# Performance work log

Hardware: AMD Instinct MI355X
Metric: run time of the kernel (lower is better)

The kernel has to match this reference:

```python
import jax, jax.numpy as jnp
import numpy as np


def setup_inputs() -> dict:
    key = jax.random.key(0)
    n_keypoints = 129          # n keypoints -> 128 segments
    spacing = 32               # uniform keypoint spacing -> m = 4096
    dim = 256
    batch = 32
    index = jnp.arange(n_keypoints, dtype=jnp.int64 if jax.config.jax_enable_x64 else jnp.int32) * spacing
    value = jax.random.normal(key, (batch, n_keypoints, dim), dtype=jnp.float32)
    return {"index": index, "value": value}


def reference(index, value):
    """Piecewise linear interpolation; vectorized over all segments/points.

    index: (n,) sorted keypoint positions (static values).
    value: (..., n, dim) keypoint values.
    returns: (..., m, dim) with m = index[-1] - index[0]; excludes the start point.
    """
    idx = index - index[0]                       # (n,) starts at 0
    m = int(np.asarray(idx)[-1])                 # static: index is a known tensor
    p = jnp.arange(1, m + 1)                     # output positions (m,)
    # segment k such that idx[k] < p <= idx[k+1]
    seg = jnp.searchsorted(idx, p, side="left") - 1   # (m,)
    x0 = idx[seg]                                # (m,)
    x1 = idx[seg + 1]                            # (m,)
    w = ((p - x0) / (x1 - x0)).astype(value.dtype)    # (m,) fractional position in segment
    y0 = value[..., seg, :]                      # (..., m, dim)
    y1 = value[..., seg + 1, :]                  # (..., m, dim)
    return y0 + (y1 - y0) * w[:, None]
```

## Files before the change

kernel.cpp:

```cpp
#include <hip/hip_runtime.h>
#include <hip/hip_bf16.h>


#define DIM 256
#define VEC_PER_ROW (DIM / 4)
#define MAX_N 256

__global__ __launch_bounds__(256) void lpi_kernel(
    const int* __restrict__ index,
    const float* __restrict__ value,
    float* __restrict__ out,
    int n, int m, int batch)
{
    __shared__ int s_idx[MAX_N];

    int base = index[0];
    for (int i = threadIdx.x; i < n; i += blockDim.x) {
        s_idx[i] = index[i] - base;
    }
    __syncthreads();

    int t = blockIdx.x * blockDim.x + threadIdx.x;
    int total = batch * m * VEC_PER_ROW;
    if (t >= total) return;

    int dv  = t & (VEC_PER_ROW - 1);
    int row = t >> 6;
    int r   = row % m;
    int b   = row / m;
    int p   = r + 1;

    int lo = 0, hi = n - 1;
    while (lo < hi) {
        int mid = (lo + hi + 1) >> 1;
        if (s_idx[mid] < p) lo = mid; else hi = mid - 1;
    }
    int seg = lo;

    int x0 = s_idx[seg];
    int x1 = s_idx[seg + 1];
    float w = (float)(p - x0) / (float)(x1 - x0);

    const float4* y0 = (const float4*)(value + (size_t)(b * n + seg) * DIM);
    const float4* y1 = y0 + VEC_PER_ROW;

    float4 a = y0[dv];
    float4 c = y1[dv];

    float4 o;
    o.x = a.x + (c.x - a.x) * w;
    o.y = a.y + (c.y - a.y) * w;
    o.z = a.z + (c.z - a.z) * w;
    o.w = a.w + (c.w - a.w) * w;

    float4* op = (float4*)(out + (size_t)(b * m + r) * DIM);
    op[dv] = o;
}

extern "C" void kernel_launch(void* const* d_in, const int* in_sizes, int n_in,
                              void* d_out, int out_size, void* d_ws, size_t ws_size,
                              hipStream_t stream) {
    const int*   index = (const int*)d_in[0];
    const float* value = (const float*)d_in[1];
    float*       out   = (float*)d_out;

    int n  = in_sizes[0];
    int bd = in_sizes[1] / n;
    const int dim = DIM;
    int batch = bd / dim;
    int m = out_size / bd;

    int total = batch * m * VEC_PER_ROW;
    int block = 256;
    int grid  = (total + block - 1) / block;

    lpi_kernel<<<grid, block, 0, stream>>>(index, value, out, n, m, batch);
}
```

Measured before the change: 162.5 us.

## Map blocks to segments, drop binary search, reuse keypoint rows with nontemporal stores

Each block now owns one (batch, segment) pair and loops over all output rows in that segment. It loads the two keypoint rows once per block and skips the per-thread binary search and the shared-memory index staging. Output is written with nontemporal stores to avoid polluting the cache. Parallelism per block now depends on segment length, so very uneven keypoint spacing could cause load imbalance.

```diff
diff --git a/kernel.cpp b/kernel.cpp
--- a/kernel.cpp
+++ b/kernel.cpp
@@ -4,57 +4,42 @@
 
 #define DIM 256
 #define VEC_PER_ROW (DIM / 4)
-#define MAX_N 256
+
+typedef float vfloat4 __attribute__((ext_vector_type(4)));
 
 __global__ __launch_bounds__(256) void lpi_kernel(
     const int* __restrict__ index,
     const float* __restrict__ value,
     float* __restrict__ out,
-    int n, int m, int batch)
+    int n, int m)
 {
-    __shared__ int s_idx[MAX_N];
+    int nseg = n - 1;
+    int seg  = blockIdx.x % nseg;
+    int b    = blockIdx.x / nseg;
 
     int base = index[0];
-    for (int i = threadIdx.x; i < n; i += blockDim.x) {
-        s_idx[i] = index[i] - base;
+    int x0   = index[seg]     - base;
+    int x1   = index[seg + 1] - base;
+    int len  = x1 - x0;
+
+    int lane = threadIdx.x & 63;
+    int wv   = threadIdx.x >> 6;
+
+    const vfloat4* y0 = (const vfloat4*)(value + (size_t)(b * n + seg) * DIM);
+    const vfloat4* y1 = y0 + VEC_PER_ROW;
+
+    vfloat4 a = y0[lane];
+    vfloat4 c = y1[lane];
+    vfloat4 d = c - a;
+
+    float flen = (float)len;
+
+    for (int k = wv; k < len; k += 4) {
+        float w = (float)(k + 1) / flen;
+        vfloat4 o = a + d * w;
+        vfloat4* op = (vfloat4*)(out + (size_t)(b * m + x0 + k) * DIM);
+        __builtin_nontemporal_store(o, op + lane);
     }
-    __syncthreads();
-
-    int t = blockIdx.x * blockDim.x + threadIdx.x;
-    int total = batch * m * VEC_PER_ROW;
-    if (t >= total) return;
-
-    int dv  = t & (VEC_PER_ROW - 1);
-    int row = t >> 6;
-    int r   = row % m;
-    int b   = row / m;
-    int p   = r + 1;
-
-    int lo = 0, hi = n - 1;
-    while (lo < hi) {
-        int mid = (lo + hi + 1) >> 1;
-        if (s_idx[mid] < p) lo = mid; else hi = mid - 1;
-    }
-    int seg = lo;
-
-    int x0 = s_idx[seg];
-    int x1 = s_idx[seg + 1];
-    float w = (float)(p - x0) / (float)(x1 - x0);
-
-    const float4* y0 = (const float4*)(value + (size_t)(b * n + seg) * DIM);
-    const float4* y1 = y0 + VEC_PER_ROW;
-
-    float4 a = y0[dv];
-    float4 c = y1[dv];
-
-    float4 o;
-    o.x = a.x + (c.x - a.x) * w;
-    o.y = a.y + (c.y - a.y) * w;
-    o.z = a.z + (c.z - a.z) * w;
-    o.w = a.w + (c.w - a.w) * w;
-
-    float4* op = (float4*)(out + (size_t)(b * m + r) * DIM);
-    op[dv] = o;
 }
 
 extern "C" void kernel_launch(void* const* d_in, const int* in_sizes, int n_in,
@@ -70,9 +55,6 @@
     int batch = bd / dim;
     int m = out_size / bd;
 
-    int total = batch * m * VEC_PER_ROW;
-    int block = 256;
-    int grid  = (total + block - 1) / block;
-
-    lpi_kernel<<<grid, block, 0, stream>>>(index, value, out, n, m, batch);
+    int grid = batch * (n - 1);
+    lpi_kernel<<<grid, 256, 0, stream>>>(index, value, out, n, m);
 }
```

After: 144.2 us. 1.13x faster.
